# Optimization experiments

Measured on AMD Instinct MI355X. Metric: run time of the kernel, lower is better.

The kernel has to match this reference:

```python
import jax, jax.numpy as jnp
import numpy as np

B, S, D = 2, 2048, 1024
H = 16
HD = D // H  # 64

def setup_inputs() -> dict:
    key = jax.random.key(0)
    ks = jax.random.split(key, 6)
    scale = 0.02
    x   = jax.random.normal(ks[0], (B, S, D), dtype=jnp.float32)
    Wq  = jax.random.normal(ks[1], (D, D), dtype=jnp.float32) * scale
    Wk  = jax.random.normal(ks[2], (D, D), dtype=jnp.float32) * scale
    Wv  = jax.random.normal(ks[3], (D, D), dtype=jnp.float32) * scale
    Wo  = jax.random.normal(ks[4], (D, D), dtype=jnp.float32) * scale
    bo  = jax.random.normal(ks[5], (D,), dtype=jnp.float32) * scale
    return {"x": x, "Wq": Wq, "Wk": Wk, "Wv": Wv, "Wo": Wo, "bo": bo}

def reference(x, Wq, Wk, Wv, Wo, bo):
    b, s, d = x.shape
    # QKV projections (no bias, qkv_bias=False); weights stored as [d_in, d_out]
    q = (x @ Wq).reshape(b, s, H, HD).transpose(0, 2, 1, 3)  # [b,h,s,hd]
    k = (x @ Wk).reshape(b, s, H, HD).transpose(0, 2, 1, 3)
    v = (x @ Wv).reshape(b, s, H, HD).transpose(0, 2, 1, 3)
    scores = jnp.einsum('bhqd,bhkd->bhqk', q, k)  # [b,h,s,s]
    causal = jnp.triu(jnp.ones((s, s), dtype=bool), k=1)
    scores = jnp.where(causal, -jnp.inf, scores)
    attn = jax.nn.softmax(scores / jnp.sqrt(jnp.float32(HD)), axis=-1)
    # dropout_rate = 0.0 -> identity
    ctx = jnp.einsum('bhqk,bhkd->bqhd', attn, v).reshape(b, s, d)
    return ctx @ Wo + bo
```

## Files before the change

kernel.cpp:

```cpp
#include <hip/hip_runtime.h>
#include <hip/hip_bf16.h>
#include <math.h>

#define B_ 2
#define S_ 2048
#define D_ 1024
#define H_ 16
#define HD_ 64
#define M_ (B_*S_)

typedef __attribute__((ext_vector_type(8))) short bf16x8;
typedef __attribute__((ext_vector_type(4))) float f32x4;

#define MFMA16(a,b,c) __builtin_amdgcn_mfma_f32_16x16x32_bf16(a,b,c,0,0,0)
#define INFF __builtin_inff()
#define LOG2E 1.44269504088896340736f
#define EXP2F(x) __builtin_amdgcn_exp2f(x)

static __device__ __forceinline__ unsigned short f2bf_bits(float f) {
    unsigned int u = __float_as_uint(f);
    unsigned int r = (u + 0x7fffu + ((u >> 16) & 1u)) >> 16;
    return (unsigned short)r;
}

static __device__ __forceinline__ unsigned cvt_pk_bf16(float a, float b) {
    unsigned r;
    asm("v_cvt_pk_bf16_f32 %0, %1, %2" : "=v"(r) : "v"(a), "v"(b));
    return r;
}

static __device__ __forceinline__ void gload16(const unsigned short* g, unsigned short* l) {
    __builtin_amdgcn_global_load_lds(
        (const __attribute__((address_space(1))) unsigned int*)(g),
        (__attribute__((address_space(3))) unsigned int*)(l),
        16, 0, 0);
}

#define PH_WAIT_BAR(N) do { \
    asm volatile("s_waitcnt vmcnt(" #N ")" ::: "memory"); \
    __builtin_amdgcn_sched_barrier(0); \
    __builtin_amdgcn_s_barrier(); \
    __builtin_amdgcn_sched_barrier(0); \
} while (0)
#define PH_BAR do { \
    __builtin_amdgcn_sched_barrier(0); \
    __builtin_amdgcn_s_barrier(); \
    __builtin_amdgcn_sched_barrier(0); \
} while (0)

__global__ __launch_bounds__(256) void convert_x_kernel(
    const float* __restrict__ x, unsigned short* __restrict__ o) {
    size_t i = (size_t)blockIdx.x * 256 + threadIdx.x;
    float4 v = reinterpret_cast<const float4*>(x)[i];
    ushort4 u;
    u.x = f2bf_bits(v.x); u.y = f2bf_bits(v.y);
    u.z = f2bf_bits(v.z); u.w = f2bf_bits(v.w);
    reinterpret_cast<ushort4*>(o)[i] = u;
}

__global__ __launch_bounds__(256) void convw_kernel(
    const float* __restrict__ W0, const float* __restrict__ W1,
    const float* __restrict__ W2, const float* __restrict__ W3,
    unsigned short* __restrict__ OT) {
    __shared__ float t[32][33];
    const float* W = (blockIdx.z == 0) ? W0 : (blockIdx.z == 1) ? W1
                    : (blockIdx.z == 2) ? W2 : W3;
    unsigned short* O = OT + (size_t)blockIdx.z * D_ * D_;
    int tx = threadIdx.x & 31, ty = threadIdx.x >> 5;
    int kb = blockIdx.y * 32, nb = blockIdx.x * 32;
#pragma unroll
    for (int i = 0; i < 4; i++)
        t[ty + 8*i][tx] = W[(size_t)(kb + ty + 8*i) * D_ + nb + tx];
    __syncthreads();
#pragma unroll
    for (int i = 0; i < 4; i++) {
        int n = nb + ty + 8*i, k = kb + tx;
        O[(size_t)n * D_ + k] = f2bf_bits(t[tx][ty + 8*i]);
    }
}

__global__ __launch_bounds__(512, 2) void gemm_qkv256(
    const unsigned short* __restrict__ A,
    const unsigned short* __restrict__ BT,
    unsigned short* __restrict__ outp)
{
    __shared__ union {
        struct { unsigned short A[2][2][8192]; unsigned short B[2][2][8192]; } s;
        unsigned short vt[256][136];
    } sm;
    const int tid = threadIdx.x, lane = tid & 63, wid = tid >> 6;
    const int lrow = lane & 15, lk8 = lane >> 4, orow = lk8 * 4;
    const int wmo = (wid >> 2) * 64;
    const int wno = (wid & 3) * 32;
    const int m0 = blockIdx.x * 256, n0 = blockIdx.y * 256;

    const int srow = lane >> 3, sgr = lane & 7;
    const unsigned sgo = (unsigned)(wid * 8 + srow) * 1024u
                       + (unsigned)((sgr ^ srow) << 3);
    const unsigned short* Ag = A  + (unsigned)m0 * 1024u + sgo;
    const unsigned short* Bg = BT + (unsigned)n0 * 1024u + sgo;
    const int ldsrb = wid * 512;

    const int sw0 = ((lk8 ^ (lrow & 7)) << 3);
    const int sw1 = (((4 | lk8) ^ (lrow & 7)) << 3);
    int ar[4], br[2];
#pragma unroll
    for (int f = 0; f < 4; f++) ar[f] = (wmo + f * 16 + lrow) * 64;
#pragma unroll
    for (int g = 0; g < 2; g++) br[g] = (wno + g * 16 + lrow) * 64;

    f32x4 acc[8][4] = {};
    bf16x8 af[4][2], bf[2][2];

    auto stA = [&](int par, int mh, unsigned k) {
        unsigned short* d = &sm.s.A[par][mh][ldsrb];
        const unsigned short* g = Ag + (unsigned)mh * 131072u + k;
        gload16(g, d);
        gload16(g + 65536u, d + 4096);
    };
    auto stB = [&](int par, int nh, unsigned k) {
        unsigned short* d = &sm.s.B[par][nh][ldsrb];
        const unsigned short* g = Bg + (unsigned)nh * 131072u + k;
        gload16(g, d);
        gload16(g + 65536u, d + 4096);
    };
    auto lda = [&](int par, int qm) {
        const unsigned short* p = &sm.s.A[par][qm][0];
#pragma unroll
        for (int f = 0; f < 4; f++) {
            af[f][0] = *reinterpret_cast<const bf16x8*>(p + ar[f] + sw0);
            af[f][1] = *reinterpret_cast<const bf16x8*>(p + ar[f] + sw1);
        }
    };
    auto ldb = [&](int par, int qn) {
        const unsigned short* p = &sm.s.B[par][qn][0];
#pragma unroll
        for (int g = 0; g < 2; g++) {
            bf[g][0] = *reinterpret_cast<const bf16x8*>(p + br[g] + sw0);
            bf[g][1] = *reinterpret_cast<const bf16x8*>(p + br[g] + sw1);
        }
    };
    auto mma = [&](int qm, int qn) {
        __builtin_amdgcn_s_setprio(1);
#pragma unroll
        for (int f = 0; f < 4; f++)
#pragma unroll
            for (int g = 0; g < 2; g++)
#pragma unroll
                for (int ks = 0; ks < 2; ks++)
                    acc[qm*4+f][qn*2+g] =
                        MFMA16(af[f][ks], bf[g][ks], acc[qm*4+f][qn*2+g]);
        __builtin_amdgcn_s_setprio(0);
    };

    stB(0, 0, 0); stA(0, 0, 0); stB(0, 1, 0); stA(0, 1, 0);
    PH_WAIT_BAR(4);

#pragma unroll 1
    for (int t = 0; t < 16; t++) {
        const int par = t & 1, pn = par ^ 1;
        const unsigned kn = (t < 15) ? (unsigned)(t + 1) * 64u : 0u;
        lda(par, 0); ldb(par, 0);
        stB(pn, 0, kn); stA(pn, 0, kn); stB(pn, 1, kn); stA(pn, 1, kn);
        mma(0, 0);  PH_WAIT_BAR(10);
        ldb(par, 1);  mma(0, 1);  PH_WAIT_BAR(8);
        lda(par, 1);  mma(1, 1);  PH_BAR;
        ldb(par, 0);  mma(1, 0);  PH_WAIT_BAR(4);
    }

    asm volatile("s_waitcnt vmcnt(0)" ::: "memory");
    __builtin_amdgcn_sched_barrier(0);
    __builtin_amdgcn_s_barrier();

    const int which = n0 >> 10;
    const int nl0 = n0 & 1023;
    const int bq = m0 >> 11;
    unsigned short* obase = outp + (size_t)which * 4194304;

    if (which < 2) {
        const float scale = (which == 0) ? (0.125f * LOG2E) : 1.0f;
#pragma unroll
        for (int fi = 0; fi < 8; fi++)
#pragma unroll
            for (int g = 0; g < 4; g++)
#pragma unroll
                for (int r = 0; r < 4; r++) {
                    int m = m0 + (fi >> 2) * 128 + wmo + (fi & 3) * 16 + orow + r;
                    int n = nl0 + (g >> 1) * 128 + wno + (g & 1) * 16 + lrow;
                    int s = m & 2047;
                    obase[(((size_t)(bq * 16 + (n >> 6)) * 2048 + s) << 6) + (n & 63)]
                        = f2bf_bits(acc[fi][g][r] * scale);
                }
    } else {
#pragma unroll
        for (int qm = 0; qm < 2; qm++) {
#pragma unroll
            for (int f = 0; f < 4; f++)
#pragma unroll
                for (int g = 0; g < 4; g++) {
                    const int ml = wmo + f * 16 + orow;
                    const int nc = (g >> 1) * 128 + wno + (g & 1) * 16 + lrow;
                    uint2 w;
                    w.x = cvt_pk_bf16(acc[qm*4+f][g][0], acc[qm*4+f][g][1]);
                    w.y = cvt_pk_bf16(acc[qm*4+f][g][2], acc[qm*4+f][g][3]);
                    *reinterpret_cast<uint2*>(&sm.vt[nc][ml]) = w;
                }
            __syncthreads();
            {
                const int row = tid >> 1, c0 = (tid & 1) * 64;
                unsigned short* dst = obase +
                    ((size_t)(bq * 1024) + nl0 + row) * 2048 +
                    (m0 & 2047) + qm * 128 + c0;
#pragma unroll
                for (int j = 0; j < 64; j += 8)
                    *reinterpret_cast<bf16x8*>(dst + j) =
                        *reinterpret_cast<const bf16x8*>(&sm.vt[row][c0 + j]);
            }
            __syncthreads();
        }
    }
}

template<int BN, int MODE>
__global__ __launch_bounds__(256) void gemm_gl(
    const unsigned short* __restrict__ A,
    const unsigned short* __restrict__ BT,
    void* __restrict__ outp,
    const float* __restrict__ bias)
{
    constexpr int K = 1024;
    constexpr int NF = (BN == 128) ? 4 : 2;
    __shared__ struct { unsigned short As[128][64]; unsigned short Bs[BN][64]; } sm;
    const int m0 = blockIdx.x * 128;
    const int n0 = blockIdx.y * BN;
    const int tid = threadIdx.x, lane = tid & 63, wid = tid >> 6;
    const int wm = (wid >> 1) * 64;
    const int wn = (wid & 1) * (BN / 2);
    const int lrow = lane & 15, lk8 = lane >> 4, orow = lk8 * 4;
    f32x4 acc[4][NF] = {};

    for (int k0 = 0; k0 < K; k0 += 64) {
#pragma unroll
        for (int i = 0; i < 4; i++) {
            const int rbase = wid * 32 + i * 8;
            const int rl = rbase + (lane >> 3);
            const int sc = ((lane & 7) ^ (rl & 7)) << 3;
            gload16(A + (size_t)(m0 + rl) * K + k0 + sc, &sm.As[rbase][0]);
        }
#pragma unroll
        for (int i = 0; i < BN / 32; i++) {
            const int rbase = wid * (BN / 4) + i * 8;
            const int rl = rbase + (lane >> 3);
            const int sc = ((lane & 7) ^ (rl & 7)) << 3;
            gload16(BT + (size_t)(n0 + rl) * K + k0 + sc, &sm.Bs[rbase][0]);
        }
        __syncthreads();
#pragma unroll
        for (int ks = 0; ks < 2; ks++) {
            bf16x8 af[4], bfr[NF];
#pragma unroll
            for (int f = 0; f < 4; f++) {
                const int row = wm + f * 16 + lrow;
                const int p = (ks * 4 + lk8) ^ (row & 7);
                af[f] = *reinterpret_cast<const bf16x8*>(&sm.As[row][p * 8]);
            }
#pragma unroll
            for (int f = 0; f < NF; f++) {
                const int row = wn + f * 16 + lrow;
                const int p = (ks * 4 + lk8) ^ (row & 7);
                bfr[f] = *reinterpret_cast<const bf16x8*>(&sm.Bs[row][p * 8]);
            }
            __builtin_amdgcn_s_setprio(1);
#pragma unroll
            for (int mf = 0; mf < 4; mf++)
#pragma unroll
                for (int nf = 0; nf < NF; nf++)
                    acc[mf][nf] = MFMA16(af[mf], bfr[nf], acc[mf][nf]);
            __builtin_amdgcn_s_setprio(0);
        }
        __syncthreads();
    }

    float* o = (float*)outp;
#pragma unroll
    for (int mf = 0; mf < 4; mf++)
#pragma unroll
        for (int nf = 0; nf < NF; nf++)
#pragma unroll
            for (int r = 0; r < 4; r++) {
                int m = m0 + wm + mf*16 + orow + r;
                int n = n0 + wn + nf*16 + lrow;
                o[(size_t)m * 1024 + n] = acc[mf][nf][r] + bias[n];
            }
}

__global__ __launch_bounds__(256, 4) void attn_kernel(
    const unsigned short* __restrict__ Q,
    const unsigned short* __restrict__ Kb,
    const unsigned short* __restrict__ VT,
    unsigned short* __restrict__ ctx)
{
    __shared__ unsigned short Ks[2][64][64];
    __shared__ unsigned short Vs[2][64][64];
    __shared__ unsigned short Pl[4][16][64];
    const int fid = blockIdx.x;
    const int xcd = fid & 7, t = fid >> 3;
    const int bh = xcd | ((t & 3) << 3);
    const int qt = 31 - (t >> 2);
    const int lane = threadIdx.x & 63, wid = threadIdx.x >> 6;
    const int lrow = lane & 15, lk8 = lane >> 4, orow = lk8 * 4;
    const unsigned short* Qp = Q  + (size_t)bh * (S_ * 64);
    const unsigned short* Kp = Kb + (size_t)bh * (S_ * 64);
    const unsigned short* Vp = VT + (size_t)bh * (64 * S_);
    const int b = bh >> 4, h = bh & 15;
    const int q0 = qt * 64 + wid * 16;
    const int nb = qt + 1;
    const int psw = (lrow & 7) << 3;

    auto stage = [&](int buf, int kv0) {
#pragma unroll
        for (int i = 0; i < 2; i++) {
            const int rbase = wid * 16 + 8 * i;
            const int rl = rbase + (lane >> 3);
            const int sc = (((lane & 7) ^ (rl & 7)) << 3);
            gload16(Kp + (size_t)(kv0 + rl) * 64 + sc, &Ks[buf][rbase][0]);
            gload16(Vp + (size_t)rl * S_ + kv0 + sc, &Vs[buf][rbase][0]);
        }
    };

    stage(0, 0);

    bf16x8 qf[2];
#pragma unroll
    for (int kt = 0; kt < 2; kt++)
        qf[kt] = *reinterpret_cast<const bf16x8*>(
            Qp + (size_t)(q0 + lrow) * 64 + kt*32 + lk8*8);

    f32x4 acc[4] = {};
    float lr = 0.f;

    __syncthreads();

#pragma unroll 1
    for (int kvb = 0; kvb < nb; kvb++) {
        const int cur = kvb & 1;
        if (kvb + 1 < nb) stage(cur ^ 1, (kvb + 1) * 64);

        f32x4 sacc[4] = {};
        __builtin_amdgcn_s_setprio(1);
#pragma unroll
        for (int kt = 0; kt < 2; kt++)
#pragma unroll
            for (int nf = 0; nf < 4; nf++) {
                const int row = nf * 16 + lrow;
                const int g = ((kt << 2) | lk8) ^ (row & 7);
                bf16x8 kf = *reinterpret_cast<const bf16x8*>(&Ks[cur][row][g << 3]);
                sacc[nf] = MFMA16(kf, qf[kt], sacc[nf]);
            }
        __builtin_amdgcn_s_setprio(0);
        if (kvb == qt) {
#pragma unroll
            for (int nf = 0; nf < 4; nf++)
#pragma unroll
                for (int r = 0; r < 4; r++)
                    if (nf*16 + orow + r > wid*16 + lrow) sacc[nf][r] = -INFF;
        }
        float ps[4];
#pragma unroll
        for (int nf = 0; nf < 4; nf++) {
#pragma unroll
            for (int r = 0; r < 4; r++)
                sacc[nf][r] = EXP2F(sacc[nf][r]);
            ps[nf] = (sacc[nf][0] + sacc[nf][1]) + (sacc[nf][2] + sacc[nf][3]);
        }
        lr += (ps[0] + ps[1]) + (ps[2] + ps[3]);
#pragma unroll
        for (int nf = 0; nf < 4; nf++) {
            uint2 w;
            w.x = cvt_pk_bf16(sacc[nf][0], sacc[nf][1]);
            w.y = cvt_pk_bf16(sacc[nf][2], sacc[nf][3]);
            *reinterpret_cast<uint2*>(&Pl[wid][lrow][(nf*16 + orow) ^ psw]) = w;
        }
        bf16x8 pf[2];
#pragma unroll
        for (int kt = 0; kt < 2; kt++)
            pf[kt] = *reinterpret_cast<const bf16x8*>(
                &Pl[wid][lrow][(kt*32 + lk8*8) ^ psw]);
        __builtin_amdgcn_s_setprio(1);
#pragma unroll
        for (int kt = 0; kt < 2; kt++)
#pragma unroll
            for (int nf = 0; nf < 4; nf++) {
                const int row = nf * 16 + lrow;
                const int g = ((kt << 2) | lk8) ^ (row & 7);
                bf16x8 vf = *reinterpret_cast<const bf16x8*>(&Vs[cur][row][g << 3]);
                acc[nf] = MFMA16(pf[kt], vf, acc[nf]);
            }
        __builtin_amdgcn_s_setprio(0);
        __syncthreads();
    }

    lr += __shfl_xor(lr, 16);
    lr += __shfl_xor(lr, 32);
    const float inv = 1.0f / lr;
#pragma unroll
    for (int r = 0; r < 4; r++) {
        const float linv = __shfl(inv, (lane & 48) + orow + r);
#pragma unroll
        for (int nf = 0; nf < 4; nf++) {
            int s = q0 + orow + r;
            int col = h * 64 + nf * 16 + lrow;
            ctx[((size_t)(b * S_ + s)) * D_ + col] = f2bf_bits(acc[nf][r] * linv);
        }
    }
}

extern "C" void kernel_launch(void* const* d_in, const int* in_sizes, int n_in,
                              void* d_out, int out_size, void* d_ws, size_t ws_size,
                              hipStream_t stream) {
    const float* x  = (const float*)d_in[0];
    const float* Wq = (const float*)d_in[1];
    const float* Wk = (const float*)d_in[2];
    const float* Wv = (const float*)d_in[3];
    const float* Wo = (const float*)d_in[4];
    const float* bo = (const float*)d_in[5];
    float* out = (float*)d_out;

    char* ws = (char*)d_ws;
    unsigned short* xb  = (unsigned short*)(ws);
    unsigned short* WT  = (unsigned short*)(ws + 8388608);
    unsigned short* QKV = (unsigned short*)(ws + 16777216);
    unsigned short* ctx = (unsigned short*)(ws + 41943040);

    unsigned short* Qb  = QKV;
    unsigned short* Kb  = QKV + 4194304;
    unsigned short* VTb = QKV + 8388608;

    convert_x_kernel<<<dim3(4096), dim3(256), 0, stream>>>(x, xb);
    convw_kernel<<<dim3(32, 32, 4), dim3(256), 0, stream>>>(Wq, Wk, Wv, Wo, WT);

    gemm_qkv256<<<dim3(16, 12), dim3(512), 0, stream>>>(xb, WT, QKV);

    attn_kernel<<<dim3(1024), dim3(256), 0, stream>>>(Qb, Kb, VTb, ctx);

    gemm_gl<64, 1><<<dim3(32, 16), dim3(256), 0, stream>>>(
        ctx, WT + 3145728, (void*)out, bo);
}
```

Baseline: 102.0 us.

## Restructure QKV GEMM main loop into 8-phase ping-pong with finer LDS waits

Rewrites the K-loop of the projection GEMM as an unrolled two-stage body that issues global-to-LDS loads for upcoming K-steps at quarter-tile granularity, interleaved with MFMA phases. It keeps two separate B fragment register sets and uses explicit lgkmcnt/vmcnt waits with barriers around each MFMA block. The aim is to hide global load latency and LDS reads better behind matrix math. The cost is more barriers per iteration and higher register pressure, which may reduce occupancy.

```diff
diff --git a/kernel.cpp b/kernel.cpp
--- a/kernel.cpp
+++ b/kernel.cpp
@@ -36,15 +36,21 @@
         16, 0, 0);
 }
 
-#define PH_WAIT_BAR(N) do { \
-    asm volatile("s_waitcnt vmcnt(" #N ")" ::: "memory"); \
+#define BARR do { \
     __builtin_amdgcn_sched_barrier(0); \
     __builtin_amdgcn_s_barrier(); \
     __builtin_amdgcn_sched_barrier(0); \
 } while (0)
-#define PH_BAR do { \
+#define LGK0 do { \
+    asm volatile("s_waitcnt lgkmcnt(0)" ::: "memory"); \
     __builtin_amdgcn_sched_barrier(0); \
-    __builtin_amdgcn_s_barrier(); \
+} while (0)
+#define LGK8 do { \
+    asm volatile("s_waitcnt lgkmcnt(8)" ::: "memory"); \
+    __builtin_amdgcn_sched_barrier(0); \
+} while (0)
+#define VM6 do { \
+    asm volatile("s_waitcnt vmcnt(6)" ::: "memory"); \
     __builtin_amdgcn_sched_barrier(0); \
 } while (0)
 
@@ -110,7 +116,7 @@
     for (int g = 0; g < 2; g++) br[g] = (wno + g * 16 + lrow) * 64;
 
     f32x4 acc[8][4] = {};
-    bf16x8 af[4][2], bf[2][2];
+    bf16x8 af[4][2], bf0[2][2], bf1[2][2];
 
     auto stA = [&](int par, int mh, unsigned k) {
         unsigned short* d = &sm.s.A[par][mh][ldsrb];
@@ -124,23 +130,31 @@
         gload16(g, d);
         gload16(g + 65536u, d + 4096);
     };
-    auto lda = [&](int par, int qm) {
-        const unsigned short* p = &sm.s.A[par][qm][0];
+    auto lda = [&](int par, int mh) {
+        const unsigned short* p = &sm.s.A[par][mh][0];
 #pragma unroll
         for (int f = 0; f < 4; f++) {
             af[f][0] = *reinterpret_cast<const bf16x8*>(p + ar[f] + sw0);
             af[f][1] = *reinterpret_cast<const bf16x8*>(p + ar[f] + sw1);
         }
     };
-    auto ldb = [&](int par, int qn) {
-        const unsigned short* p = &sm.s.B[par][qn][0];
+    auto ldb0 = [&](int par, int nh) {
+        const unsigned short* p = &sm.s.B[par][nh][0];
 #pragma unroll
         for (int g = 0; g < 2; g++) {
-            bf[g][0] = *reinterpret_cast<const bf16x8*>(p + br[g] + sw0);
-            bf[g][1] = *reinterpret_cast<const bf16x8*>(p + br[g] + sw1);
-        }
-    };
-    auto mma = [&](int qm, int qn) {
+            bf0[g][0] = *reinterpret_cast<const bf16x8*>(p + br[g] + sw0);
+            bf0[g][1] = *reinterpret_cast<const bf16x8*>(p + br[g] + sw1);
+        }
+    };
+    auto ldb1 = [&](int par, int nh) {
+        const unsigned short* p = &sm.s.B[par][nh][0];
+#pragma unroll
+        for (int g = 0; g < 2; g++) {
+            bf1[g][0] = *reinterpret_cast<const bf16x8*>(p + br[g] + sw0);
+            bf1[g][1] = *reinterpret_cast<const bf16x8*>(p + br[g] + sw1);
+        }
+    };
+    auto MMA0 = [&](int mh) {
         __builtin_amdgcn_s_setprio(1);
 #pragma unroll
         for (int f = 0; f < 4; f++)
@@ -148,24 +162,46 @@
             for (int g = 0; g < 2; g++)
 #pragma unroll
                 for (int ks = 0; ks < 2; ks++)
-                    acc[qm*4+f][qn*2+g] =
-                        MFMA16(af[f][ks], bf[g][ks], acc[qm*4+f][qn*2+g]);
+                    acc[mh*4+f][g] = MFMA16(af[f][ks], bf0[g][ks], acc[mh*4+f][g]);
         __builtin_amdgcn_s_setprio(0);
     };
-
-    stB(0, 0, 0); stA(0, 0, 0); stB(0, 1, 0); stA(0, 1, 0);
-    PH_WAIT_BAR(4);
+    auto MMA1 = [&](int mh) {
+        __builtin_amdgcn_s_setprio(1);
+#pragma unroll
+        for (int f = 0; f < 4; f++)
+#pragma unroll
+            for (int g = 0; g < 2; g++)
+#pragma unroll
+                for (int ks = 0; ks < 2; ks++)
+                    acc[mh*4+f][2+g] = MFMA16(af[f][ks], bf1[g][ks], acc[mh*4+f][2+g]);
+        __builtin_amdgcn_s_setprio(0);
+    };
+
+    stA(0, 0, 0);  stB(0, 0, 0);  stB(0, 1, 0);  stA(0, 1, 0);
+    stA(1, 0, 64); stB(1, 0, 64); stB(1, 1, 64);
+    VM6; BARR;
 
 #pragma unroll 1
-    for (int t = 0; t < 16; t++) {
-        const int par = t & 1, pn = par ^ 1;
-        const unsigned kn = (t < 15) ? (unsigned)(t + 1) * 64u : 0u;
-        lda(par, 0); ldb(par, 0);
-        stB(pn, 0, kn); stA(pn, 0, kn); stB(pn, 1, kn); stA(pn, 1, kn);
-        mma(0, 0);  PH_WAIT_BAR(10);
-        ldb(par, 1);  mma(0, 1);  PH_WAIT_BAR(8);
-        lda(par, 1);  mma(1, 1);  PH_BAR;
-        ldb(par, 0);  mma(1, 0);  PH_WAIT_BAR(4);
+    for (int i = 0; i < 8; i++) {
+        const unsigned kA1 = (unsigned)(2*i + 1) * 64u;
+        const unsigned k2  = (unsigned)((2*i + 2) & 15) * 64u;
+        const unsigned k3  = (unsigned)((2*i + 3) & 15) * 64u;
+        lda(0, 0); ldb0(0, 0); stA(1, 1, kA1);
+        LGK8; BARR; LGK0; MMA0(0); BARR;
+        ldb1(0, 1); stA(0, 0, k2);
+        BARR; LGK0; MMA1(0); BARR;
+        lda(0, 1); stB(0, 0, k2);
+        BARR; LGK0; MMA1(1); BARR;
+        stB(0, 1, k2);
+        VM6; BARR; MMA0(1); BARR;
+        lda(1, 0); ldb0(1, 0); stA(0, 1, k2);
+        LGK8; BARR; LGK0; MMA0(0); BARR;
+        ldb1(1, 1); stA(1, 0, k3);
+        BARR; LGK0; MMA1(0); BARR;
+        lda(1, 1); stB(1, 0, k3);
+        BARR; LGK0; MMA1(1); BARR;
+        stB(1, 1, k3);
+        VM6; BARR; MMA0(1); BARR;
     }
 
     asm volatile("s_waitcnt vmcnt(0)" ::: "memory");
```

Measured after the change: 99.48 us. 1.03x faster.
